# Kernel tuning notes

Hardware: AMD Instinct MI355X
Metric: run time of the kernel (lower is better)

## Reference

```python
import jax, jax.numpy as jnp
import numpy as np

N_NODES = 50000
N_EDGES = 600000
D_IN = 128
D_HID = 1024
D_OUT = 128


def setup_inputs() -> dict:
    key = jax.random.key(0)
    ks = jax.random.split(key, 8)
    feat = jax.random.normal(ks[0], (N_NODES, D_IN), dtype=jnp.float32)
    edge_feat = jax.random.normal(ks[1], (N_EDGES, D_IN), dtype=jnp.float32)
    src = jax.random.randint(ks[2], (N_EDGES,), 0, N_NODES, dtype=jnp.int32)
    dst = jax.random.randint(ks[3], (N_EDGES,), 0, N_NODES, dtype=jnp.int32)
    W1 = jax.random.normal(ks[4], (D_IN, D_HID), dtype=jnp.float32) * (1.0 / np.sqrt(D_IN))
    b1 = jnp.zeros((D_HID,), dtype=jnp.float32)
    W2 = jax.random.normal(ks[5], (D_HID, D_OUT), dtype=jnp.float32) * (1.0 / np.sqrt(D_HID))
    b2 = jnp.zeros((D_OUT,), dtype=jnp.float32)
    return {"feat": feat, "edge_feat": edge_feat, "src": src, "dst": dst,
            "W1": W1, "b1": b1, "W2": W2, "b2": b2}


def reference(feat, edge_feat, src, dst, W1, b1, W2, b2):
    # DGL u_add_e: message m_e = h_src(e) + e_feat(e)   [E, D_IN]
    messages = feat[src] + edge_feat
    # reduce sum over incoming edges at each destination node -> [N, D_IN]
    h = jax.ops.segment_sum(messages, dst, num_segments=N_NODES)
    # 2-layer MLP
    h = jax.nn.relu(h @ W1 + b1)
    return h @ W2 + b2
```

## Files before the change

kernel.cpp:

```cpp
#include <hip/hip_runtime.h>
#include <hip/hip_bf16.h>

#define N_NODES 50000
#define N_EDGES 600000
#define D_IN    128
#define D_HID   1024
#define D_OUT   128

#define WS_H      0
#define WS_PAIRS  12800000
#define WS_OFF    17600000
#define WS_CURSOR 17800016
#define WS_DEG    18000016
#define WS_BSUM   18200016
#define WS_W1T    18201040
#define WS_W2T    18463184

typedef short bf16x8 __attribute__((ext_vector_type(8)));
typedef float f32x4  __attribute__((ext_vector_type(4)));
typedef int   i32x2  __attribute__((ext_vector_type(2)));

__global__ __launch_bounds__(256) void hist_kernel(
    const int* __restrict__ dst, int* __restrict__ deg)
{
    int e = blockIdx.x * blockDim.x + threadIdx.x;
    if (e < N_EDGES) atomicAdd(&deg[dst[e]], 1);
}

__global__ __launch_bounds__(256) void scan1_kernel(
    const int* __restrict__ deg, int* __restrict__ bsum)
{
    __shared__ int red[256];
    int t = threadIdx.x;
    int idx = blockIdx.x * 256 + t;
    red[t] = (idx < N_NODES) ? deg[idx] : 0;
    __syncthreads();
    for (int s = 128; s > 0; s >>= 1) {
        if (t < s) red[t] += red[t + s];
        __syncthreads();
    }
    if (t == 0) bsum[blockIdx.x] = red[0];
}

#define SCAN_NB 196
__global__ __launch_bounds__(256) void scan2_kernel(
    int* __restrict__ bsum, int* __restrict__ off)
{
    __shared__ int sh[256];
    int t = threadIdx.x;
    int v = (t < SCAN_NB) ? bsum[t] : 0;
    sh[t] = v;
    __syncthreads();
    for (int ofs = 1; ofs < 256; ofs <<= 1) {
        int u = (t >= ofs) ? sh[t - ofs] : 0;
        __syncthreads();
        sh[t] += u;
        __syncthreads();
    }
    if (t < SCAN_NB) bsum[t] = sh[t] - v;
    if (t == 255) off[N_NODES] = sh[255];
}

__global__ __launch_bounds__(256) void scan3_kernel(
    const int* __restrict__ deg, const int* __restrict__ bsum,
    int* __restrict__ off, int* __restrict__ cursor)
{
    __shared__ int sh[256];
    int t = threadIdx.x;
    int idx = blockIdx.x * 256 + t;
    int v = (idx < N_NODES) ? deg[idx] : 0;
    sh[t] = v;
    __syncthreads();
    for (int ofs = 1; ofs < 256; ofs <<= 1) {
        int u = (t >= ofs) ? sh[t - ofs] : 0;
        __syncthreads();
        sh[t] += u;
        __syncthreads();
    }
    if (idx < N_NODES) {
        int ex = bsum[blockIdx.x] + sh[t] - v;
        off[idx] = ex;
        cursor[idx] = ex;
    }
}

__global__ __launch_bounds__(256) void fill_kernel(
    const int* __restrict__ dst, const int* __restrict__ src,
    int* __restrict__ cursor, int* __restrict__ pairs)
{
    int e = blockIdx.x * blockDim.x + threadIdx.x;
    if (e < N_EDGES) {
        int s = src[e];
        int pos = atomicAdd(&cursor[dst[e]], 1);
        i32x2 v; v.x = e; v.y = s;
        *(i32x2*)(pairs + 2 * (size_t)pos) = v;
    }
}

__global__ __launch_bounds__(256) void transpose_cvt2_kernel(
    const float* __restrict__ W1, __hip_bfloat16* __restrict__ w1t,
    const float* __restrict__ W2, __hip_bfloat16* __restrict__ w2t)
{
    __shared__ float tile[32][33];
    int b = blockIdx.x;
    const float* in;
    __hip_bfloat16* outp;
    int rows, cols, c0, r0;
    if (b < 128) {
        in = W1; outp = w1t; rows = D_IN; cols = D_HID;
        c0 = (b & 31) * 32; r0 = (b >> 5) * 32;
    } else {
        int bb = b - 128;
        in = W2; outp = w2t; rows = D_HID; cols = D_OUT;
        c0 = (bb & 3) * 32; r0 = (bb >> 2) * 32;
    }
    int tx = threadIdx.x & 31, ty = threadIdx.x >> 5;
    #pragma unroll
    for (int i = 0; i < 32; i += 8)
        tile[ty + i][tx] = in[(size_t)(r0 + ty + i) * cols + (c0 + tx)];
    __syncthreads();
    #pragma unroll
    for (int i = 0; i < 32; i += 8)
        outp[(size_t)(c0 + ty + i) * rows + (r0 + tx)] =
            __float2bfloat16(tile[tx][ty + i]);
}

__global__ __launch_bounds__(256) void gather_kernel(
    const float* __restrict__ feat,
    const float* __restrict__ edge_feat,
    const int*   __restrict__ pairs,
    const int*   __restrict__ off,
    __hip_bfloat16* __restrict__ hbf)
{
    const int wv   = threadIdx.x >> 6;
    const int lane = threadIdx.x & 63;
    const int n = blockIdx.x * 4 + wv;
    if (n >= N_NODES) return;

    int i   = __builtin_amdgcn_readfirstlane(off[n]);
    int end = __builtin_amdgcn_readfirstlane(off[n + 1]);

    float2 a0 = make_float2(0.f, 0.f), a1 = a0, a2 = a0, a3 = a0;

    for (; i + 8 <= end; i += 8) {
        i32x2 p0 = *(const i32x2*)(pairs + 2 * (size_t)(i + 0));
        i32x2 p1 = *(const i32x2*)(pairs + 2 * (size_t)(i + 1));
        i32x2 p2 = *(const i32x2*)(pairs + 2 * (size_t)(i + 2));
        i32x2 p3 = *(const i32x2*)(pairs + 2 * (size_t)(i + 3));
        i32x2 p4 = *(const i32x2*)(pairs + 2 * (size_t)(i + 4));
        i32x2 p5 = *(const i32x2*)(pairs + 2 * (size_t)(i + 5));
        i32x2 p6 = *(const i32x2*)(pairs + 2 * (size_t)(i + 6));
        i32x2 p7 = *(const i32x2*)(pairs + 2 * (size_t)(i + 7));
        float2 e0 = ((const float2*)(edge_feat + (size_t)p0.x * D_IN))[lane];
        float2 g0 = ((const float2*)(feat      + (size_t)p0.y * D_IN))[lane];
        float2 e1 = ((const float2*)(edge_feat + (size_t)p1.x * D_IN))[lane];
        float2 g1 = ((const float2*)(feat      + (size_t)p1.y * D_IN))[lane];
        float2 e2 = ((const float2*)(edge_feat + (size_t)p2.x * D_IN))[lane];
        float2 g2 = ((const float2*)(feat      + (size_t)p2.y * D_IN))[lane];
        float2 e3 = ((const float2*)(edge_feat + (size_t)p3.x * D_IN))[lane];
        float2 g3 = ((const float2*)(feat      + (size_t)p3.y * D_IN))[lane];
        float2 e4 = ((const float2*)(edge_feat + (size_t)p4.x * D_IN))[lane];
        float2 g4 = ((const float2*)(feat      + (size_t)p4.y * D_IN))[lane];
        float2 e5 = ((const float2*)(edge_feat + (size_t)p5.x * D_IN))[lane];
        float2 g5 = ((const float2*)(feat      + (size_t)p5.y * D_IN))[lane];
        float2 e6 = ((const float2*)(edge_feat + (size_t)p6.x * D_IN))[lane];
        float2 g6 = ((const float2*)(feat      + (size_t)p6.y * D_IN))[lane];
        float2 e7 = ((const float2*)(edge_feat + (size_t)p7.x * D_IN))[lane];
        float2 g7 = ((const float2*)(feat      + (size_t)p7.y * D_IN))[lane];
        a0.x += e0.x + g0.x;  a0.y += e0.y + g0.y;
        a1.x += e1.x + g1.x;  a1.y += e1.y + g1.y;
        a2.x += e2.x + g2.x;  a2.y += e2.y + g2.y;
        a3.x += e3.x + g3.x;  a3.y += e3.y + g3.y;
        a0.x += e4.x + g4.x;  a0.y += e4.y + g4.y;
        a1.x += e5.x + g5.x;  a1.y += e5.y + g5.y;
        a2.x += e6.x + g6.x;  a2.y += e6.y + g6.y;
        a3.x += e7.x + g7.x;  a3.y += e7.y + g7.y;
    }
    for (; i + 2 <= end; i += 2) {
        i32x2 p0 = *(const i32x2*)(pairs + 2 * (size_t)(i + 0));
        i32x2 p1 = *(const i32x2*)(pairs + 2 * (size_t)(i + 1));
        float2 e0 = ((const float2*)(edge_feat + (size_t)p0.x * D_IN))[lane];
        float2 g0 = ((const float2*)(feat      + (size_t)p0.y * D_IN))[lane];
        float2 e1 = ((const float2*)(edge_feat + (size_t)p1.x * D_IN))[lane];
        float2 g1 = ((const float2*)(feat      + (size_t)p1.y * D_IN))[lane];
        a0.x += e0.x + g0.x;  a0.y += e0.y + g0.y;
        a1.x += e1.x + g1.x;  a1.y += e1.y + g1.y;
    }
    if (i < end) {
        i32x2 p = *(const i32x2*)(pairs + 2 * (size_t)i);
        float2 e = ((const float2*)(edge_feat + (size_t)p.x * D_IN))[lane];
        float2 g = ((const float2*)(feat      + (size_t)p.y * D_IN))[lane];
        a0.x += e.x + g.x;  a0.y += e.y + g.y;
    }
    float sx = (a0.x + a1.x) + (a2.x + a3.x);
    float sy = (a0.y + a1.y) + (a2.y + a3.y);
    __hip_bfloat162 hv;
    hv.x = __float2bfloat16(sx);
    hv.y = __float2bfloat16(sy);
    ((__hip_bfloat162*)(hbf + (size_t)n * D_IN))[lane] = hv;
}

#define HS_STRIDE 136
#define QS_STRIDE 72

__global__ __launch_bounds__(256) void mlp_mfma_kernel(
    const __hip_bfloat16* __restrict__ hbf,
    const __hip_bfloat16* __restrict__ w1t,
    const float* __restrict__ b1,
    const __hip_bfloat16* __restrict__ w2t,
    const float* __restrict__ b2,
    float* __restrict__ out)
{
    __shared__ __align__(16) short h_s[64 * HS_STRIDE];
    __shared__ __align__(16) short q_s[2][64 * QS_STRIDE];

    const int t    = threadIdx.x;
    const int wv   = t >> 6;
    const int lane = t & 63;
    const int half = lane >> 4;
    const int lid  = lane & 15;
    const int nb   = blockIdx.x * 64;

    const short* hs  = (const short*)hbf;
    const short* w1s = (const short*)w1t;
    const short* w2s = (const short*)w2t;

    for (int u = t; u < 64 * 16; u += 256) {
        int r = u >> 4, c = u & 15;
        int row = nb + r;
        uint4 v = make_uint4(0u, 0u, 0u, 0u);
        if (row < N_NODES) v = ((const uint4*)(hs + (size_t)row * 128))[c];
        *(uint4*)&h_s[r * HS_STRIDE + c * 8] = v;
    }
    __syncthreads();

    bf16x8 afrag[4][4];
    #pragma unroll
    for (int mt = 0; mt < 4; ++mt)
        #pragma unroll
        for (int ks = 0; ks < 4; ++ks)
            afrag[mt][ks] = *(const bf16x8*)&h_s[(mt * 16 + lid) * HS_STRIDE + ks * 32 + half * 8];

    f32x4 acc[4][2];
    #pragma unroll
    for (int mt = 0; mt < 4; ++mt) {
        acc[mt][0] = f32x4{0.f, 0.f, 0.f, 0.f};
        acc[mt][1] = f32x4{0.f, 0.f, 0.f, 0.f};
    }

    const int ncol1 = wv * 16 + lid;

    int pb = 0;
    for (int jb = 0; jb < D_HID; jb += 64, pb ^= 1) {
        float bias = b1[jb + ncol1];
        bf16x8 bfrag[4];
        #pragma unroll
        for (int ks = 0; ks < 4; ++ks)
            bfrag[ks] = *(const bf16x8*)&w1s[(size_t)(jb + ncol1) * 128 + ks * 32 + half * 8];

        f32x4 c1[4];
        #pragma unroll
        for (int mt = 0; mt < 4; ++mt) {
            f32x4 c = f32x4{bias, bias, bias, bias};
            #pragma unroll
            for (int ks = 0; ks < 4; ++ks)
                c = __builtin_amdgcn_mfma_f32_16x16x32_bf16(afrag[mt][ks], bfrag[ks], c, 0, 0, 0);
            c1[mt] = c;
        }

        #pragma unroll
        for (int mt = 0; mt < 4; ++mt) {
            #pragma unroll
            for (int r = 0; r < 4; ++r) {
                float v = fmaxf(c1[mt][r], 0.f);
                __hip_bfloat16 bv = __float2bfloat16(v);
                q_s[pb][(mt * 16 + half * 4 + r) * QS_STRIDE + wv * 16 + lid] = *(short*)&bv;
            }
        }
        __syncthreads();

        bf16x8 a2f[4][2];
        #pragma unroll
        for (int mt = 0; mt < 4; ++mt)
            #pragma unroll
            for (int ks = 0; ks < 2; ++ks)
                a2f[mt][ks] = *(const bf16x8*)&q_s[pb][(mt * 16 + lid) * QS_STRIDE + ks * 32 + half * 8];

        #pragma unroll
        for (int nt = 0; nt < 2; ++nt) {
            #pragma unroll
            for (int ks = 0; ks < 2; ++ks) {
                bf16x8 b2f = *(const bf16x8*)&w2s[(size_t)(wv * 32 + nt * 16 + lid) * 1024 + jb + ks * 32 + half * 8];
                #pragma unroll
                for (int mt = 0; mt < 4; ++mt)
                    acc[mt][nt] = __builtin_amdgcn_mfma_f32_16x16x32_bf16(a2f[mt][ks], b2f, acc[mt][nt], 0, 0, 0);
            }
        }
    }

    #pragma unroll
    for (int nt = 0; nt < 2; ++nt) {
        int col = wv * 32 + nt * 16 + lid;
        float bv = b2[col];
        #pragma unroll
        for (int mt = 0; mt < 4; ++mt) {
            #pragma unroll
            for (int r = 0; r < 4; ++r) {
                int row = nb + mt * 16 + half * 4 + r;
                if (row < N_NODES)
                    out[(size_t)row * D_OUT + col] = acc[mt][nt][r] + bv;
            }
        }
    }
}

extern "C" void kernel_launch(void* const* d_in, const int* in_sizes, int n_in,
                              void* d_out, int out_size, void* d_ws, size_t ws_size,
                              hipStream_t stream) {
    const float* feat      = (const float*)d_in[0];
    const float* edge_feat = (const float*)d_in[1];
    const int*   src       = (const int*)d_in[2];
    const int*   dst       = (const int*)d_in[3];
    const float* W1        = (const float*)d_in[4];
    const float* b1        = (const float*)d_in[5];
    const float* W2        = (const float*)d_in[6];
    const float* b2        = (const float*)d_in[7];
    float* out = (float*)d_out;

    char* ws = (char*)d_ws;
    __hip_bfloat16* hbf = (__hip_bfloat16*)(ws + WS_H);
    int*   pairs  = (int*)(ws + WS_PAIRS);
    int*   off    = (int*)(ws + WS_OFF);
    int*   cursor = (int*)(ws + WS_CURSOR);
    int*   deg    = (int*)(ws + WS_DEG);
    int*   bsum   = (int*)(ws + WS_BSUM);
    __hip_bfloat16* w1t = (__hip_bfloat16*)(ws + WS_W1T);
    __hip_bfloat16* w2t = (__hip_bfloat16*)(ws + WS_W2T);

    hipMemsetAsync(deg, 0, (size_t)N_NODES * sizeof(int), stream);

    hist_kernel<<<(N_EDGES + 255) / 256, 256, 0, stream>>>(dst, deg);
    scan1_kernel<<<SCAN_NB, 256, 0, stream>>>(deg, bsum);
    scan2_kernel<<<1, 256, 0, stream>>>(bsum, off);
    scan3_kernel<<<SCAN_NB, 256, 0, stream>>>(deg, bsum, off, cursor);
    fill_kernel<<<(N_EDGES + 255) / 256, 256, 0, stream>>>(dst, src, cursor, pairs);

    transpose_cvt2_kernel<<<256, 256, 0, stream>>>(W1, w1t, W2, w2t);

    gather_kernel<<<(N_NODES + 3) / 4, 256, 0, stream>>>(
        feat, edge_feat, pairs, off, hbf);

    mlp_mfma_kernel<<<(N_NODES + 63) / 64, 256, 0, stream>>>(
        hbf, w1t, b1, w2t, b2, out);
}
```

Before: 611.6 us.

## Restructure MLP kernel: direct h fragment loads, transposed GEMM1, 128-wide hidden chunks

The MLP kernel no longer stages h in shared memory. Each wave loads its h fragments straight from global memory into registers, clamping rows past the end instead of zero-filling. The first GEMM is transposed (W1 as the A operand, h as B), so each lane writes four contiguous bf16 outputs as one vector store into shared memory. The hidden dimension is now processed in 128-wide chunks, which halves the number of barriers per block but doubles the q_s buffer and the per-iteration register footprint.

```diff
diff --git a/kernel.cpp b/kernel.cpp
--- a/kernel.cpp
+++ b/kernel.cpp
@@ -17,6 +17,7 @@
 #define WS_W2T    18463184
 
 typedef short bf16x8 __attribute__((ext_vector_type(8)));
+typedef short s16x4  __attribute__((ext_vector_type(4)));
 typedef float f32x4  __attribute__((ext_vector_type(4)));
 typedef int   i32x2  __attribute__((ext_vector_type(2)));
 
@@ -200,8 +201,7 @@
     ((__hip_bfloat162*)(hbf + (size_t)n * D_IN))[lane] = hv;
 }
 
-#define HS_STRIDE 136
-#define QS_STRIDE 72
+#define QS_STRIDE 136
 
 __global__ __launch_bounds__(256) void mlp_mfma_kernel(
     const __hip_bfloat16* __restrict__ hbf,
@@ -211,7 +211,6 @@
     const float* __restrict__ b2,
     float* __restrict__ out)
 {
-    __shared__ __align__(16) short h_s[64 * HS_STRIDE];
     __shared__ __align__(16) short q_s[2][64 * QS_STRIDE];
 
     const int t    = threadIdx.x;
@@ -225,21 +224,15 @@
     const short* w1s = (const short*)w1t;
     const short* w2s = (const short*)w2t;
 
-    for (int u = t; u < 64 * 16; u += 256) {
-        int r = u >> 4, c = u & 15;
-        int row = nb + r;
-        uint4 v = make_uint4(0u, 0u, 0u, 0u);
-        if (row < N_NODES) v = ((const uint4*)(hs + (size_t)row * 128))[c];
-        *(uint4*)&h_s[r * HS_STRIDE + c * 8] = v;
-    }
-    __syncthreads();
-
-    bf16x8 afrag[4][4];
-    #pragma unroll
-    for (int mt = 0; mt < 4; ++mt)
+    bf16x8 hfrag[4][4];
+    #pragma unroll
+    for (int nt = 0; nt < 4; ++nt) {
+        int row = nb + nt * 16 + lid;
+        if (row >= N_NODES) row = N_NODES - 1;
         #pragma unroll
         for (int ks = 0; ks < 4; ++ks)
-            afrag[mt][ks] = *(const bf16x8*)&h_s[(mt * 16 + lid) * HS_STRIDE + ks * 32 + half * 8];
+            hfrag[nt][ks] = *(const bf16x8*)&hs[(size_t)row * 128 + ks * 32 + half * 8];
+    }
 
     f32x4 acc[4][2];
     #pragma unroll
@@ -248,52 +241,51 @@
         acc[mt][1] = f32x4{0.f, 0.f, 0.f, 0.f};
     }
 
-    const int ncol1 = wv * 16 + lid;
-
     int pb = 0;
-    for (int jb = 0; jb < D_HID; jb += 64, pb ^= 1) {
-        float bias = b1[jb + ncol1];
-        bf16x8 bfrag[4];
+    for (int jb = 0; jb < D_HID; jb += 128, pb ^= 1) {
         #pragma unroll
-        for (int ks = 0; ks < 4; ++ks)
-            bfrag[ks] = *(const bf16x8*)&w1s[(size_t)(jb + ncol1) * 128 + ks * 32 + half * 8];
-
-        f32x4 c1[4];
-        #pragma unroll
-        for (int mt = 0; mt < 4; ++mt) {
-            f32x4 c = f32x4{bias, bias, bias, bias};
+        for (int ht = 0; ht < 2; ++ht) {
+            const int hid0 = jb + wv * 32 + ht * 16;
+            bf16x8 w1f[4];
             #pragma unroll
             for (int ks = 0; ks < 4; ++ks)
-                c = __builtin_amdgcn_mfma_f32_16x16x32_bf16(afrag[mt][ks], bfrag[ks], c, 0, 0, 0);
-            c1[mt] = c;
-        }
-
-        #pragma unroll
-        for (int mt = 0; mt < 4; ++mt) {
-            #pragma unroll
-            for (int r = 0; r < 4; ++r) {
-                float v = fmaxf(c1[mt][r], 0.f);
-                __hip_bfloat16 bv = __float2bfloat16(v);
-                q_s[pb][(mt * 16 + half * 4 + r) * QS_STRIDE + wv * 16 + lid] = *(short*)&bv;
+                w1f[ks] = *(const bf16x8*)&w1s[(size_t)(hid0 + lid) * 128 + ks * 32 + half * 8];
+            f32x4 bias4 = *(const f32x4*)&b1[hid0 + half * 4];
+            #pragma unroll
+            for (int nt = 0; nt < 4; ++nt) {
+                f32x4 c = bias4;
+                #pragma unroll
+                for (int ks = 0; ks < 4; ++ks)
+                    c = __builtin_amdgcn_mfma_f32_16x16x32_bf16(w1f[ks], hfrag[nt][ks], c, 0, 0, 0);
+                s16x4 hv;
+                #pragma unroll
+                for (int r = 0; r < 4; ++r) {
+                    float v = fmaxf(c[r], 0.f);
+                    __hip_bfloat16 bv = __float2bfloat16(v);
+                    hv[r] = *(short*)&bv;
+                }
+                *(s16x4*)&q_s[pb][(nt * 16 + lid) * QS_STRIDE + wv * 32 + ht * 16 + half * 4] = hv;
             }
         }
         __syncthreads();
 
-        bf16x8 a2f[4][2];
         #pragma unroll
-        for (int mt = 0; mt < 4; ++mt)
-            #pragma unroll
-            for (int ks = 0; ks < 2; ++ks)
-                a2f[mt][ks] = *(const bf16x8*)&q_s[pb][(mt * 16 + lid) * QS_STRIDE + ks * 32 + half * 8];
-
-        #pragma unroll
-        for (int nt = 0; nt < 2; ++nt) {
-            #pragma unroll
-            for (int ks = 0; ks < 2; ++ks) {
-                bf16x8 b2f = *(const bf16x8*)&w2s[(size_t)(wv * 32 + nt * 16 + lid) * 1024 + jb + ks * 32 + half * 8];
+        for (int kh = 0; kh < 2; ++kh) {
+            bf16x8 a2f[4][2];
+            #pragma unroll
+            for (int mt = 0; mt < 4; ++mt)
                 #pragma unroll
-                for (int mt = 0; mt < 4; ++mt)
-                    acc[mt][nt] = __builtin_amdgcn_mfma_f32_16x16x32_bf16(a2f[mt][ks], b2f, acc[mt][nt], 0, 0, 0);
+                for (int ks = 0; ks < 2; ++ks)
+                    a2f[mt][ks] = *(const bf16x8*)&q_s[pb][(mt * 16 + lid) * QS_STRIDE + kh * 64 + ks * 32 + half * 8];
+            #pragma unroll
+            for (int nt = 0; nt < 2; ++nt) {
+                #pragma unroll
+                for (int ks = 0; ks < 2; ++ks) {
+                    bf16x8 b2f = *(const bf16x8*)&w2s[(size_t)(wv * 32 + nt * 16 + lid) * 1024 + jb + kh * 64 + ks * 32 + half * 8];
+                    #pragma unroll
+                    for (int mt = 0; mt < 4; ++mt)
+                        acc[mt][nt] = __builtin_amdgcn_mfma_f32_16x16x32_bf16(a2f[mt][ks], b2f, acc[mt][nt], 0, 0, 0);
+                }
             }
         }
     }
```

Measured after the change: 605.3 us. About the same (-1.0%).
